# Kernel tuning notes

Hardware: AMD Instinct MI355X
Metric: run time of the kernel (lower is better)

Reference implementation:

```python
import jax, jax.numpy as jnp
import numpy as np

N_NODES = 50000
IN_F = 128
OUT_F = 128
N_EDGES = 800000
ALPHA = 0.2  # LeakyReLU negative slope
EPS = 1e-16

def _xavier(key, shape, gain=1.414):
    fan_in, fan_out = shape[0], shape[1]
    bound = gain * np.sqrt(6.0 / (fan_in + fan_out))
    return jax.random.uniform(key, shape, jnp.float32, -bound, bound)

def setup_inputs() -> dict:
    key = jax.random.key(0)
    k_h, k_e, k_W, k_a = jax.random.split(key, 4)
    h = jax.random.normal(k_h, (N_NODES, IN_F), dtype=jnp.float32)
    edge_index = jax.random.randint(k_e, (2, N_EDGES), 0, N_NODES, dtype=jnp.int64)
    W = _xavier(k_W, (IN_F, OUT_F))
    a = _xavier(k_a, (2 * OUT_F, 1))
    return {"h": h, "edge_index": edge_index, "W": W, "a": a}

def reference(h, edge_index, W, a):
    # h: [N, F_in], edge_index: [2, E], W: [F_in, F_out], a: [2*F_out, 1]
    Wh = h @ W                                   # [N, F_out]
    row, col = edge_index[0], edge_index[1]
    # cat([Wh_i, Wh_j]) @ a  ==  Wh_i @ a1 + Wh_j @ a2  (compute per-node, gather per-edge)
    a1, a2 = a[:OUT_F, 0], a[OUT_F:, 0]
    s1 = Wh @ a1                                 # [N]
    s2 = Wh @ a2                                 # [N]
    e = jax.nn.leaky_relu(s1[row] + s2[col], negative_slope=ALPHA)  # [E]
    # NOTE: original code's "e_rowmax" is actually a segment SUM (index_add_), replicated faithfully
    e_rowsum = jax.ops.segment_sum(e, row, num_segments=N_NODES)    # [N]
    e_exp = jnp.exp(e - e_rowsum[row])                              # [E]
    e_exp_sum = jax.ops.segment_sum(e_exp, row, num_segments=N_NODES)
    attention = e_exp / (e_exp_sum[row] + EPS)                      # [E]
    # weighted scatter-add aggregation
    h_prime = jax.ops.segment_sum(attention[:, None] * Wh[col], row, num_segments=N_NODES)
    return h_prime
```

## Files before the change

### kernel.cpp

```cpp
#include <hip/hip_runtime.h>
#include <hip/hip_bf16.h>
#include <math.h>

#define NNODES 50000
#define NF 128
#define NEDGES 800000
#define ALPHA 0.2f
#define EPS 1e-16f
#define EPT 2
#define GEMM_BLOCKS 782
#define EDGE_BLOCKS 1563
#define CAP 64

typedef __attribute__((ext_vector_type(8))) short bf16x8;
typedef __attribute__((ext_vector_type(4))) float f32x4;

__device__ inline unsigned bf16rne(float x) {
    unsigned u = __float_as_uint(x);
    return (u + 0x7FFFu + ((u >> 16) & 1u)) >> 16;
}
__device__ inline float bflo(unsigned u) { return __uint_as_float(u << 16); }
__device__ inline float bfhi(unsigned u) { return __uint_as_float(u & 0xFFFF0000u); }

__global__ __launch_bounds__(256) void prep(const float* __restrict__ W,
                                            const float* __restrict__ a,
                                            ushort* __restrict__ WbF,
                                            float* __restrict__ Wa1,
                                            float* __restrict__ Wa2,
                                            int* __restrict__ count) {
    if (blockIdx.x < 8) {
        int s = blockIdx.x * 256 + threadIdx.x;
        int l = s & 63;
        int ct = (s >> 6) & 7;
        int ks = s >> 9;
        int c = ct * 16 + (l & 15);
        int g = l >> 4;
        ushort v[8];
        #pragma unroll
        for (int j = 0; j < 8; ++j) {
            int k = ks * 32 + ((j >> 2) << 4) + g * 4 + (j & 3);
            v[j] = (ushort)bf16rne(W[k * NF + c]);
        }
        *(uint4*)&WbF[(size_t)s * 8] = *(uint4*)v;
    } else if (blockIdx.x == 8) {
        int k = threadIdx.x;
        if (k < NF) {
            float t1 = 0.f, t2 = 0.f;
            for (int c = 0; c < NF; ++c) {
                float w = W[k * NF + c];
                t1 += w * a[c];
                t2 += w * a[NF + c];
            }
            Wa1[k] = t1;
            Wa2[k] = t2;
        }
    } else {
        const int stride = (gridDim.x - 9) * 256;
        for (int i = (blockIdx.x - 9) * 256 + threadIdx.x; i < NNODES; i += stride)
            count[i] = 0;
    }
}

__global__ __launch_bounds__(256) void gemm_mfma(const float* __restrict__ h,
                                                 const ushort* __restrict__ WbF,
                                                 const float* __restrict__ Wa1,
                                                 const float* __restrict__ Wa2,
                                                 ushort* __restrict__ WhBu,
                                                 float* __restrict__ s1,
                                                 float* __restrict__ s2) {
    __shared__ ushort ldsB[16384];
    const int tid = threadIdx.x;

    #pragma unroll
    for (int i = 0; i < 8; ++i) {
        int off8 = (tid + i * 256) * 8;
        *(uint4*)&ldsB[off8] = *(const uint4*)&WbF[off8];
    }
    __syncthreads();

    const int lane = tid & 63;
    const int wrow = tid >> 6;
    const int m = lane & 15;
    const int g = lane >> 4;
    const int row = blockIdx.x * 64 + wrow * 16 + m;
    const int rowc = (row < NNODES) ? row : 0;

    f32x4 acc[8];
    #pragma unroll
    for (int t = 0; t < 8; ++t) acc[t] = (f32x4){0.f, 0.f, 0.f, 0.f};

    float p1 = 0.f, p2 = 0.f;
    #pragma unroll
    for (int ks = 0; ks < 4; ++ks) {
        const float4 ha = *(const float4*)&h[(size_t)rowc * NF + ks * 32 + g * 4];
        const float4 hb = *(const float4*)&h[(size_t)rowc * NF + ks * 32 + 16 + g * 4];
        const float4 wa1a = *(const float4*)&Wa1[ks * 32 + g * 4];
        const float4 wa1b = *(const float4*)&Wa1[ks * 32 + 16 + g * 4];
        const float4 wa2a = *(const float4*)&Wa2[ks * 32 + g * 4];
        const float4 wa2b = *(const float4*)&Wa2[ks * 32 + 16 + g * 4];
        p1 += ha.x * wa1a.x + ha.y * wa1a.y + ha.z * wa1a.z + ha.w * wa1a.w
            + hb.x * wa1b.x + hb.y * wa1b.y + hb.z * wa1b.z + hb.w * wa1b.w;
        p2 += ha.x * wa2a.x + ha.y * wa2a.y + ha.z * wa2a.z + ha.w * wa2a.w
            + hb.x * wa2b.x + hb.y * wa2b.y + hb.z * wa2b.z + hb.w * wa2b.w;
        bf16x8 afrag;
        afrag[0] = (short)bf16rne(ha.x);
        afrag[1] = (short)bf16rne(ha.y);
        afrag[2] = (short)bf16rne(ha.z);
        afrag[3] = (short)bf16rne(ha.w);
        afrag[4] = (short)bf16rne(hb.x);
        afrag[5] = (short)bf16rne(hb.y);
        afrag[6] = (short)bf16rne(hb.z);
        afrag[7] = (short)bf16rne(hb.w);
        #pragma unroll
        for (int ct = 0; ct < 8; ++ct) {
            bf16x8 bfrag = *(bf16x8*)&ldsB[((ks * 8 + ct) * 64 + lane) * 8];
            acc[ct] = __builtin_amdgcn_mfma_f32_16x16x32_bf16(afrag, bfrag, acc[ct], 0, 0, 0);
        }
    }

    p1 += __shfl_xor(p1, 16); p1 += __shfl_xor(p1, 32);
    p2 += __shfl_xor(p2, 16); p2 += __shfl_xor(p2, 32);
    if (g == 0 && row < NNODES) { s1[row] = p1; s2[row] = p2; }

    const int orow = blockIdx.x * 64 + wrow * 16 + g * 4;
    #pragma unroll
    for (int r = 0; r < 4; ++r) {
        int gr = orow + r;
        if (gr < NNODES) {
            #pragma unroll
            for (int ct = 0; ct < 8; ++ct)
                WhBu[(size_t)gr * NF + ct * 16 + m] = (ushort)bf16rne(acc[ct][r]);
        }
    }
}

__global__ __launch_bounds__(256) void edge_pass(const int* __restrict__ ei,
                                                 const float* __restrict__ s1,
                                                 const float* __restrict__ s2,
                                                 int* __restrict__ count,
                                                 float2* __restrict__ pair) {
    const int base = blockIdx.x * blockDim.x + threadIdx.x;
    const int stride = gridDim.x * blockDim.x;
    int idx[EPT], r[EPT], c[EPT];
    #pragma unroll
    for (int k = 0; k < EPT; ++k) {
        idx[k] = base + k * stride;
        if (idx[k] < NEDGES) {
            r[k] = ei[idx[k]];
            c[k] = ei[NEDGES + idx[k]];
        } else r[k] = -1;
    }
    float sv1[EPT], sv2[EPT];
    #pragma unroll
    for (int k = 0; k < EPT; ++k)
        if (r[k] >= 0) { sv1[k] = s1[r[k]]; sv2[k] = s2[c[k]]; }
    int rk[EPT];
    #pragma unroll
    for (int k = 0; k < EPT; ++k)
        if (r[k] >= 0) rk[k] = atomicAdd(&count[r[k]], 1);
    #pragma unroll
    for (int k = 0; k < EPT; ++k)
        if (r[k] >= 0 && rk[k] < CAP) {
            float s = sv1[k] + sv2[k];
            float ev = (s >= 0.f) ? s : ALPHA * s;
            pair[(size_t)r[k] * CAP + rk[k]] = make_float2(ev, __int_as_float(c[k]));
        }
}

__global__ __launch_bounds__(256) void aggregate(const int* __restrict__ count,
                                                 const float2* __restrict__ pair,
                                                 const unsigned* __restrict__ WhB,
                                                 float* __restrict__ out) {
    const int wid = threadIdx.x >> 6;
    const int lane = threadIdx.x & 63;
    const int row = blockIdx.x * 4 + wid;
    if (row >= NNODES) return;
    const int deg = min(count[row], CAP);
    const size_t base = (size_t)row * CAP;

    float ev = 0.f;
    int cv = 0;
    if (lane < deg) {
        float2 p = pair[base + lane];
        ev = p.x;
        cv = __float_as_int(p.y);
    }

    float rs = ev;
    #pragma unroll
    for (int off = 32; off; off >>= 1) rs += __shfl_xor(rs, off);
    float xv = (lane < deg) ? expf(ev - rs) : 0.f;
    float ds = xv;
    #pragma unroll
    for (int off = 32; off; off >>= 1) ds += __shfl_xor(ds, off);
    const float invd = 1.0f / (ds + EPS);

    float accx = 0.f, accy = 0.f;
    int j = 0;
    for (; j + 8 <= deg; j += 8) {
        int cc[8]; unsigned u[8]; float ww[8];
        #pragma unroll
        for (int k = 0; k < 8; ++k) cc[k] = __shfl(cv, j + k);
        #pragma unroll
        for (int k = 0; k < 8; ++k) u[k] = WhB[(size_t)cc[k] * 64 + lane];
        #pragma unroll
        for (int k = 0; k < 8; ++k) ww[k] = __shfl(xv, j + k);
        #pragma unroll
        for (int k = 0; k < 8; ++k) {
            float w = ww[k] * invd;
            accx += w * bflo(u[k]);
            accy += w * bfhi(u[k]);
        }
    }
    for (; j < deg; ++j) {
        int c = __shfl(cv, j);
        unsigned u = WhB[(size_t)c * 64 + lane];
        float w = __shfl(xv, j) * invd;
        accx += w * bflo(u);
        accy += w * bfhi(u);
    }
    ((float2*)out)[(size_t)row * 64 + lane] = make_float2(accx, accy);
}

extern "C" void kernel_launch(void* const* d_in, const int* in_sizes, int n_in,
                              void* d_out, int out_size, void* d_ws, size_t ws_size,
                              hipStream_t stream) {
    const float* h  = (const float*)d_in[0];
    const int*   ei = (const int*)d_in[1];
    const float* W  = (const float*)d_in[2];
    const float* a  = (const float*)d_in[3];
    float* out = (float*)d_out;

    char* ws = (char*)d_ws;
    size_t off = 0;
    auto alloc = [&](size_t bytes) -> void* {
        void* p = ws + off;
        off += (bytes + 255) & ~(size_t)255;
        return p;
    };

    unsigned* WhB   = (unsigned*)alloc((size_t)NNODES * 64 * 4);
    float2*   pair  = (float2*)alloc((size_t)NNODES * CAP * 8);
    ushort*   WbF   = (ushort*)alloc((size_t)2048 * 16);
    float*    Wa1   = (float*)alloc((size_t)NF * 4);
    float*    Wa2   = (float*)alloc((size_t)NF * 4);
    int*      count = (int*)alloc((size_t)NNODES * 4);
    float*    s1    = (float*)alloc((size_t)NNODES * 4);
    float*    s2    = (float*)alloc((size_t)NNODES * 4);

    prep<<<58, 256, 0, stream>>>(W, a, WbF, Wa1, Wa2, count);
    gemm_mfma<<<GEMM_BLOCKS, 256, 0, stream>>>(h, WbF, Wa1, Wa2, (ushort*)WhB, s1, s2);
    edge_pass<<<EDGE_BLOCKS, 256, 0, stream>>>(ei, s1, s2, count, pair);
    aggregate<<<(NNODES + 3) / 4, 256, 0, stream>>>(count, pair, WhB, out);
}
```

Baseline: 104.9 us.

## Fuse edge bucketing into GEMM launch and compute edge scores in aggregate

The edge-bucketing pass now runs as extra blocks inside the GEMM kernel, so the bucketing no longer waits for s1/s2 to be produced. It stores only column indices (4 bytes per edge instead of an 8-byte score/column pair). The LeakyReLU scores are recomputed in the aggregate kernel from s1/s2, which drops one kernel launch and overlaps the atomic-heavy scatter with the MFMA GEMM. Edges per thread go to 4 with half as many edge blocks. The cost is an extra gather of s2 per edge in aggregate, and the LDS allocation now also applies to the edge blocks, which can limit their occupancy.

```diff
diff --git a/kernel.cpp b/kernel.cpp
--- a/kernel.cpp
+++ b/kernel.cpp
@@ -7,9 +7,9 @@
 #define NEDGES 800000
 #define ALPHA 0.2f
 #define EPS 1e-16f
-#define EPT 2
+#define EPT 4
 #define GEMM_BLOCKS 782
-#define EDGE_BLOCKS 1563
+#define EDGE_BLOCKS 782
 #define CAP 64
 
 typedef __attribute__((ext_vector_type(8))) short bf16x8;
@@ -61,15 +61,43 @@
     }
 }
 
-__global__ __launch_bounds__(256) void gemm_mfma(const float* __restrict__ h,
-                                                 const ushort* __restrict__ WbF,
-                                                 const float* __restrict__ Wa1,
-                                                 const float* __restrict__ Wa2,
-                                                 ushort* __restrict__ WhBu,
-                                                 float* __restrict__ s1,
-                                                 float* __restrict__ s2) {
+__global__ __launch_bounds__(256) void gemm_scatter(const float* __restrict__ h,
+                                                    const ushort* __restrict__ WbF,
+                                                    const float* __restrict__ Wa1,
+                                                    const float* __restrict__ Wa2,
+                                                    const int* __restrict__ ei,
+                                                    ushort* __restrict__ WhBu,
+                                                    float* __restrict__ s1,
+                                                    float* __restrict__ s2,
+                                                    int* __restrict__ count,
+                                                    int* __restrict__ colbucket) {
     __shared__ ushort ldsB[16384];
     const int tid = threadIdx.x;
+
+    if (blockIdx.x < EDGE_BLOCKS) {
+        const int base = blockIdx.x * 256 + tid;
+        const int stride = EDGE_BLOCKS * 256;
+        int r[EPT], c[EPT];
+        #pragma unroll
+        for (int k = 0; k < EPT; ++k) {
+            int idx = base + k * stride;
+            if (idx < NEDGES) {
+                r[k] = ei[idx];
+                c[k] = ei[NEDGES + idx];
+            } else r[k] = -1;
+        }
+        int rk[EPT];
+        #pragma unroll
+        for (int k = 0; k < EPT; ++k)
+            if (r[k] >= 0) rk[k] = atomicAdd(&count[r[k]], 1);
+        #pragma unroll
+        for (int k = 0; k < EPT; ++k)
+            if (r[k] >= 0 && rk[k] < CAP)
+                colbucket[r[k] * CAP + rk[k]] = c[k];
+        return;
+    }
+
+    const int bid = blockIdx.x - EDGE_BLOCKS;
 
     #pragma unroll
     for (int i = 0; i < 8; ++i) {
@@ -82,7 +110,7 @@
     const int wrow = tid >> 6;
     const int m = lane & 15;
     const int g = lane >> 4;
-    const int row = blockIdx.x * 64 + wrow * 16 + m;
+    const int row = bid * 64 + wrow * 16 + m;
     const int rowc = (row < NNODES) ? row : 0;
 
     f32x4 acc[8];
@@ -122,7 +150,7 @@
     p2 += __shfl_xor(p2, 16); p2 += __shfl_xor(p2, 32);
     if (g == 0 && row < NNODES) { s1[row] = p1; s2[row] = p2; }
 
-    const int orow = blockIdx.x * 64 + wrow * 16 + g * 4;
+    const int orow = bid * 64 + wrow * 16 + g * 4;
     #pragma unroll
     for (int r = 0; r < 4; ++r) {
         int gr = orow + r;
@@ -134,41 +162,10 @@
     }
 }
 
-__global__ __launch_bounds__(256) void edge_pass(const int* __restrict__ ei,
+__global__ __launch_bounds__(256) void aggregate(const int* __restrict__ count,
+                                                 const int* __restrict__ colbucket,
                                                  const float* __restrict__ s1,
                                                  const float* __restrict__ s2,
-                                                 int* __restrict__ count,
-                                                 float2* __restrict__ pair) {
-    const int base = blockIdx.x * blockDim.x + threadIdx.x;
-    const int stride = gridDim.x * blockDim.x;
-    int idx[EPT], r[EPT], c[EPT];
-    #pragma unroll
-    for (int k = 0; k < EPT; ++k) {
-        idx[k] = base + k * stride;
-        if (idx[k] < NEDGES) {
-            r[k] = ei[idx[k]];
-            c[k] = ei[NEDGES + idx[k]];
-        } else r[k] = -1;
-    }
-    float sv1[EPT], sv2[EPT];
-    #pragma unroll
-    for (int k = 0; k < EPT; ++k)
-        if (r[k] >= 0) { sv1[k] = s1[r[k]]; sv2[k] = s2[c[k]]; }
-    int rk[EPT];
-    #pragma unroll
-    for (int k = 0; k < EPT; ++k)
-        if (r[k] >= 0) rk[k] = atomicAdd(&count[r[k]], 1);
-    #pragma unroll
-    for (int k = 0; k < EPT; ++k)
-        if (r[k] >= 0 && rk[k] < CAP) {
-            float s = sv1[k] + sv2[k];
-            float ev = (s >= 0.f) ? s : ALPHA * s;
-            pair[(size_t)r[k] * CAP + rk[k]] = make_float2(ev, __int_as_float(c[k]));
-        }
-}
-
-__global__ __launch_bounds__(256) void aggregate(const int* __restrict__ count,
-                                                 const float2* __restrict__ pair,
                                                  const unsigned* __restrict__ WhB,
                                                  float* __restrict__ out) {
     const int wid = threadIdx.x >> 6;
@@ -176,14 +173,14 @@
     const int row = blockIdx.x * 4 + wid;
     if (row >= NNODES) return;
     const int deg = min(count[row], CAP);
-    const size_t base = (size_t)row * CAP;
-
+
+    int cv = 0;
     float ev = 0.f;
-    int cv = 0;
+    if (lane < deg) cv = colbucket[row * CAP + lane];
+    const float s1r = s1[row];
     if (lane < deg) {
-        float2 p = pair[base + lane];
-        ev = p.x;
-        cv = __float_as_int(p.y);
+        float s = s1r + s2[cv];
+        ev = (s >= 0.f) ? s : ALPHA * s;
     }
 
     float rs = ev;
@@ -239,17 +236,17 @@
         return p;
     };
 
-    unsigned* WhB   = (unsigned*)alloc((size_t)NNODES * 64 * 4);
-    float2*   pair  = (float2*)alloc((size_t)NNODES * CAP * 8);
-    ushort*   WbF   = (ushort*)alloc((size_t)2048 * 16);
-    float*    Wa1   = (float*)alloc((size_t)NF * 4);
-    float*    Wa2   = (float*)alloc((size_t)NF * 4);
-    int*      count = (int*)alloc((size_t)NNODES * 4);
-    float*    s1    = (float*)alloc((size_t)NNODES * 4);
-    float*    s2    = (float*)alloc((size_t)NNODES * 4);
+    unsigned* WhB       = (unsigned*)alloc((size_t)NNODES * 64 * 4);
+    int*      colbucket = (int*)alloc((size_t)NNODES * CAP * 4);
+    ushort*   WbF       = (ushort*)alloc((size_t)2048 * 16);
+    float*    Wa1       = (float*)alloc((size_t)NF * 4);
+    float*    Wa2       = (float*)alloc((size_t)NF * 4);
+    int*      count     = (int*)alloc((size_t)NNODES * 4);
+    float*    s1        = (float*)alloc((size_t)NNODES * 4);
+    float*    s2        = (float*)alloc((size_t)NNODES * 4);
 
     prep<<<58, 256, 0, stream>>>(W, a, WbF, Wa1, Wa2, count);
-    gemm_mfma<<<GEMM_BLOCKS, 256, 0, stream>>>(h, WbF, Wa1, Wa2, (ushort*)WhB, s1, s2);
-    edge_pass<<<EDGE_BLOCKS, 256, 0, stream>>>(ei, s1, s2, count, pair);
-    aggregate<<<(NNODES + 3) / 4, 256, 0, stream>>>(count, pair, WhB, out);
-}
+    gemm_scatter<<<EDGE_BLOCKS + GEMM_BLOCKS, 256, 0, stream>>>(
+        h, WbF, Wa1, Wa2, ei, (ushort*)WhB, s1, s2, count, colbucket);
+    aggregate<<<(NNODES + 3) / 4, 256, 0, stream>>>(count, colbucket, s1, s2, WhB, out);
+}
```

New measurement: 98.00 us. -6.5%, faster.
